# Performance work log

Measured on AMD Instinct MI355X. Metric: run time of the kernel, lower is better.

Reference implementation:

```python
import jax, jax.numpy as jnp
import numpy as np

D_PROJ = 256      # core d_proj
WIN = 1536        # win_small (mid path, L<=mid_thr)
STRIDE = 384      # stride_small


def setup_inputs() -> dict:
    key = jax.random.key(0)
    ks = jax.random.split(key, 6)
    B, L, d_h, T, d_g = 4, 8192, 1024, 512, 256
    H = jax.random.normal(ks[0], (B, L, d_h), jnp.float32)
    G = jax.random.normal(ks[1], (B, T, d_g), jnp.float32)
    attn_mask = jnp.ones((B, L), dtype=bool)
    Wq_core = jax.random.normal(ks[2], (d_g, D_PROJ), jnp.float32) / np.float32(np.sqrt(d_g))
    Wk_core = jax.random.normal(ks[3], (d_h, D_PROJ), jnp.float32) / np.float32(np.sqrt(d_h))
    Wq_win = jax.random.normal(ks[4], (d_g, d_h), jnp.float32) / np.float32(np.sqrt(d_g))
    Wk_win = jax.random.normal(ks[5], (d_h, d_h), jnp.float32) / np.float32(np.sqrt(d_h))
    return dict(H=H, G=G, attn_mask=attn_mask, Wq_core=Wq_core, Wk_core=Wk_core,
                Wq_win=Wq_win, Wk_win=Wk_win)


def _core_pool(Hk, G, mask, Wq_core, Wk_core):
    # GoSpecificWattiPooling: GO-query cross-attention pooling over residues.
    q = jnp.einsum('btg,gp->btp', G, Wq_core)                 # [B,T,P]
    k = jnp.einsum('bwd,dp->bwp', Hk, Wk_core)                # [B,W,P]
    scores = jnp.einsum('btp,bwp->btw', q, k) * (D_PROJ ** -0.5)
    scores = jnp.where(mask[:, None, :], scores, jnp.float32(-1e30))
    alpha = jax.nn.softmax(scores, axis=-1)                   # over residues
    return jnp.einsum('btw,bwd->btd', alpha, Hk)              # [B,T,d_h]


def _window_starts(L, win, stride):
    starts, s = [], 0
    while s < L:
        e = min(s + win, L)
        starts.append(s)
        if e == L:
            break
        s += stride
    return starts


def reference(H, G, attn_mask, Wq_core, Wk_core, Wq_win, Wk_win):
    B, L, D = H.shape
    T = G.shape[1]
    starts = jnp.asarray(_window_starts(L, WIN, STRIDE), jnp.int32)
    q_t = jnp.einsum('btg,gd->btd', G, Wq_win)                # [B,T,D]
    scale = D ** -0.5

    def step(carry, s0):
        m, ssum, z = carry
        Hk = jax.lax.dynamic_slice_in_dim(H, s0, WIN, axis=1)
        mk = jax.lax.dynamic_slice_in_dim(attn_mask, s0, WIN, axis=1)
        Zk = _core_pool(Hk, G, mk, Wq_core, Wk_core)          # [B,T,D]
        k_w = jnp.einsum('btd,de->bte', Zk, Wk_win)
        lw = (jnp.sum(q_t * k_w, axis=-1, keepdims=True) * scale).astype(jnp.float32)
        m_new = jnp.maximum(m, lw)
        exp_m = jnp.exp(m - m_new)
        exp_w = jnp.exp(lw - m_new)
        ssum = ssum * exp_m + exp_w
        z = z * exp_m + exp_w * Zk.astype(jnp.float32)
        return (m_new, ssum, z), None

    init = (jnp.full((B, T, 1), -jnp.inf, jnp.float32),
            jnp.zeros((B, T, 1), jnp.float32),
            jnp.zeros((B, T, D), jnp.float32))
    (m, ssum, z), _ = jax.lax.scan(step, init, starts)
    return (z / (ssum + 1e-8)).astype(H.dtype)
```

## Files before the change

### kernel.cpp

```cpp
#include <hip/hip_runtime.h>
#include <math.h>

constexpr int Bb = 4;
constexpr int Lb = 8192;
constexpr int Dh = 1024;
constexpr int Tt = 512;
constexpr int Dg = 256;
constexpr int Pp = 256;
constexpr int NW = 19;

typedef unsigned short u16;
typedef __bf16 bf16x8 __attribute__((ext_vector_type(8)));
typedef float f32x4 __attribute__((ext_vector_type(4)));
typedef unsigned short us8 __attribute__((ext_vector_type(8)));

__device__ __forceinline__ u16 f2bf(float x) {
  union { float f; unsigned u; } v;
  v.f = x;
  unsigned r = v.u + 0x7FFFu + ((v.u >> 16) & 1u);
  return (u16)(r >> 16);
}
__device__ __forceinline__ float bf2f(unsigned v) {
  union { unsigned u; float f; } c;
  c.u = v << 16;
  return c.f;
}

#define GLDS16(g, l)                                                          \
  __builtin_amdgcn_global_load_lds(                                           \
      (const __attribute__((address_space(1))) void*)(g),                     \
      (__attribute__((address_space(3))) void*)(l), 16, 0, 0)

__device__ __forceinline__ void stage_ops(const u16* __restrict__ A, int lda,
                                          int bm, int kA, u16* As,
                                          const u16* __restrict__ B, int ldb,
                                          int bn, int kB, u16* Bs, int tid,
                                          int wid) {
  const int rr = tid >> 3;
  const int c16 = (tid & 7) ^ (rr & 7);
#pragma unroll
  for (int cc = 0; cc < 4; cc++) {
    const int r = cc * 64 + rr;
    GLDS16(A + (long long)(bm + r) * lda + kA + c16 * 8,
           As + cc * 4096 + wid * 512);
  }
#pragma unroll
  for (int cc = 0; cc < 4; cc++) {
    const int r = cc * 64 + rr;
    GLDS16(B + (long long)(bn + r) * ldb + kB + c16 * 8,
           Bs + cc * 4096 + wid * 512);
  }
}

template <int OB>
__global__ __launch_bounds__(512, 1) void gemm256(const u16* __restrict__ A,
                                                  const u16* __restrict__ B,
                                                  void* __restrict__ C,
                                                  int K, int lda, int ldb,
                                                  int ldc, long long sA,
                                                  long long sB, long long sC,
                                                  long long sK, int kSplit,
                                                  float alpha) {
  __shared__ u16 lds[65536];

  const int gx = gridDim.x, gy = gridDim.y;
  int flat = blockIdx.x + gx * (blockIdx.y + gy * blockIdx.z);
  const int nwg = gx * gy * (int)gridDim.z;
  const int q = nwg >> 3, r = nwg & 7;
  const int xcd = flat & 7, sub = flat >> 3;
  flat = (xcd < r ? xcd * (q + 1) : r * (q + 1) + (xcd - r) * q) + sub;
  const int bmI = flat % gx;
  const int t1 = flat / gx;
  const int bnI = t1 % gy;
  const int z = t1 / gy;

  const int b = z / kSplit, ks = z % kSplit;
  const int kLen = K / kSplit;
  const int nt = kLen >> 6;
  A += b * sA + (long long)ks * kLen;
  B += b * sB + (long long)ks * kLen;
  const long long cOff = (long long)b * sC + (long long)ks * sK;

  const int bm = bmI * 256, bn = bnI * 256;
  const int tid = threadIdx.x;
  const int wid = tid >> 6, l = tid & 63;
  const int wm = wid >> 2, wn = wid & 3;
  const int rl = l & 15, kq = l >> 4;
  const int xr = rl & 7;

  f32x4 acc[8][4];
#pragma unroll
  for (int i = 0; i < 8; i++)
#pragma unroll
    for (int j = 0; j < 4; j++) acc[i][j] = (f32x4){0.f, 0.f, 0.f, 0.f};

  stage_ops(A, lda, bm, 0, lds, B, ldb, bn, 0, lds + 32768, tid, wid);
  stage_ops(A, lda, bm, 64, lds + 16384, B, ldb, bn, 64, lds + 49152, tid, wid);
  asm volatile("s_waitcnt vmcnt(8)" ::: "memory");
  __builtin_amdgcn_s_barrier();

  for (int t = 0; t < nt; t++) {
    const int cur = t & 1;
    const u16* As = lds + cur * 16384;
    const u16* Bs = lds + 32768 + cur * 16384;
    bf16x8 a0[4][2], bb[4][2];

#pragma unroll
    for (int i = 0; i < 4; i++)
#pragma unroll
      for (int s = 0; s < 2; s++)
        a0[i][s] = *(const bf16x8*)(As + (wm * 128 + i * 16 + rl) * 64 +
                                    (((s * 4 + kq) ^ xr) << 3));
#pragma unroll
    for (int j = 0; j < 2; j++)
#pragma unroll
      for (int s = 0; s < 2; s++)
        bb[j][s] = *(const bf16x8*)(Bs + (wn * 64 + j * 16 + rl) * 64 +
                                    (((s * 4 + kq) ^ xr) << 3));
    __builtin_amdgcn_s_barrier();
    __builtin_amdgcn_s_setprio(1);
#pragma unroll
    for (int i = 0; i < 4; i++)
#pragma unroll
      for (int j = 0; j < 2; j++)
#pragma unroll
        for (int s = 0; s < 2; s++)
          acc[i][j] = __builtin_amdgcn_mfma_f32_16x16x32_bf16(
              a0[i][s], bb[j][s], acc[i][j], 0, 0, 0);
    __builtin_amdgcn_s_setprio(0);
    __builtin_amdgcn_s_barrier();

#pragma unroll
    for (int j = 2; j < 4; j++)
#pragma unroll
      for (int s = 0; s < 2; s++)
        bb[j][s] = *(const bf16x8*)(Bs + (wn * 64 + j * 16 + rl) * 64 +
                                    (((s * 4 + kq) ^ xr) << 3));
    __builtin_amdgcn_s_barrier();
    __builtin_amdgcn_s_setprio(1);
#pragma unroll
    for (int i = 0; i < 4; i++)
#pragma unroll
      for (int j = 2; j < 4; j++)
#pragma unroll
        for (int s = 0; s < 2; s++)
          acc[i][j] = __builtin_amdgcn_mfma_f32_16x16x32_bf16(
              a0[i][s], bb[j][s], acc[i][j], 0, 0, 0);
    __builtin_amdgcn_s_setprio(0);
    __builtin_amdgcn_s_barrier();

#pragma unroll
    for (int i = 0; i < 4; i++)
#pragma unroll
      for (int s = 0; s < 2; s++)
        a0[i][s] = *(const bf16x8*)(As + (wm * 128 + 64 + i * 16 + rl) * 64 +
                                    (((s * 4 + kq) ^ xr) << 3));
    __builtin_amdgcn_s_barrier();
    __builtin_amdgcn_s_setprio(1);
#pragma unroll
    for (int i = 0; i < 4; i++)
#pragma unroll
      for (int j = 2; j < 4; j++)
#pragma unroll
        for (int s = 0; s < 2; s++)
          acc[i + 4][j] = __builtin_amdgcn_mfma_f32_16x16x32_bf16(
              a0[i][s], bb[j][s], acc[i + 4][j], 0, 0, 0);
    __builtin_amdgcn_s_setprio(0);
    __builtin_amdgcn_s_barrier();

    if (t + 2 < nt) {
      u16* Asw = (u16*)lds + cur * 16384;
      u16* Bsw = (u16*)lds + 32768 + cur * 16384;
      stage_ops(A, lda, bm, (t + 2) * 64, Asw, B, ldb, bn, (t + 2) * 64, Bsw,
                tid, wid);
    }
    __builtin_amdgcn_s_setprio(1);
#pragma unroll
    for (int i = 0; i < 4; i++)
#pragma unroll
      for (int j = 0; j < 2; j++)
#pragma unroll
        for (int s = 0; s < 2; s++)
          acc[i + 4][j] = __builtin_amdgcn_mfma_f32_16x16x32_bf16(
              a0[i][s], bb[j][s], acc[i + 4][j], 0, 0, 0);
    __builtin_amdgcn_s_setprio(0);
    if (t + 2 < nt)
      asm volatile("s_waitcnt vmcnt(8)" ::: "memory");
    else
      asm volatile("s_waitcnt vmcnt(0)" ::: "memory");
    __builtin_amdgcn_s_barrier();
  }

  float* Cf = (float*)C;
  u16* Cb = (u16*)C;
#pragma unroll
  for (int i = 0; i < 8; i++) {
    const int row0 = bm + wm * 128 + i * 16 + kq * 4;
#pragma unroll
    for (int j = 0; j < 4; j++) {
      const int col = bn + wn * 64 + j * 16 + rl;
#pragma unroll
      for (int r2 = 0; r2 < 4; r2++) {
        const float v = alpha * acc[i][j][r2];
        const long long idx = cOff + (long long)(row0 + r2) * ldc + col;
        if (OB)
          Cb[idx] = f2bf(v);
        else
          Cf[idx] = v;
      }
    }
  }
}

template <int OB, int ORD>
__global__ __launch_bounds__(256) void mgemm(const u16* __restrict__ A,
                                             const u16* __restrict__ B,
                                             void* __restrict__ C,
                                             int K, int lda, int ldb, int ldc,
                                             long long sA, long long sB,
                                             long long sC, long long sK,
                                             int kSplit, float alpha) {
  __shared__ u16 smem[8192];
  u16* As = smem;
  u16* Bs = smem + 4096;

  const int gx = gridDim.x, gy = gridDim.y;
  int flat = blockIdx.x + gx * (blockIdx.y + gy * blockIdx.z);
  const int nwg = gx * gy * (int)gridDim.z;
  const int q = nwg >> 3, r = nwg & 7;
  const int xcd = flat & 7, sub = flat >> 3;
  flat = (xcd < r ? xcd * (q + 1) : r * (q + 1) + (xcd - r) * q) + sub;
  int bmI, bnI, z;
  if (ORD == 0) {
    bmI = flat % gx;
    const int t = flat / gx;
    bnI = t % gy;
    z = t / gy;
  } else {
    bnI = flat % gy;
    const int t = flat / gy;
    bmI = t % gx;
    z = t / gx;
  }

  const int b = z / kSplit, ks = z % kSplit;
  const int kLen = K / kSplit;
  A += b * sA + (long long)ks * kLen;
  B += b * sB + (long long)ks * kLen;
  const long long cOff = (long long)b * sC + (long long)ks * sK;

  const int bm = bmI * 128;
  const int bn = bnI * 128;
  const int tid = threadIdx.x;
  const int l = tid & 63;
  const int wid = tid >> 6;
  const int wm = wid >> 1, wn = wid & 1;

  const int sr = l >> 2, sj = l & 3;
  const int skb = sj ^ ((sr >> 1) & 3);

  f32x4 acc[4][4];
#pragma unroll
  for (int i = 0; i < 4; i++)
#pragma unroll
    for (int j = 0; j < 4; j++) acc[i][j] = (f32x4){0.f, 0.f, 0.f, 0.f};

  const int rl = l & 15, kb = l >> 4;

  for (int k0 = 0; k0 < kLen; k0 += 32) {
    __syncthreads();
    {
      const int c1 = wid, c2 = wid + 4;
      GLDS16(A + (long long)(bm + c1 * 16 + sr) * lda + k0 + skb * 8,
             As + c1 * 512);
      GLDS16(A + (long long)(bm + c2 * 16 + sr) * lda + k0 + skb * 8,
             As + c2 * 512);
      GLDS16(B + (long long)(bn + c1 * 16 + sr) * ldb + k0 + skb * 8,
             Bs + c1 * 512);
      GLDS16(B + (long long)(bn + c2 * 16 + sr) * ldb + k0 + skb * 8,
             Bs + c2 * 512);
    }
    __syncthreads();

    bf16x8 af[4], bfr[4];
#pragma unroll
    for (int f = 0; f < 4; f++) {
      const int rowA = wm * 64 + f * 16 + rl;
      const int unitA = rowA * 4 + (kb ^ ((rowA >> 1) & 3));
      af[f] = *(const bf16x8*)(As + unitA * 8);
      const int rowB = wn * 64 + f * 16 + rl;
      const int unitB = rowB * 4 + (kb ^ ((rowB >> 1) & 3));
      bfr[f] = *(const bf16x8*)(Bs + unitB * 8);
    }
#pragma unroll
    for (int i = 0; i < 4; i++)
#pragma unroll
      for (int j = 0; j < 4; j++)
        acc[i][j] = __builtin_amdgcn_mfma_f32_16x16x32_bf16(af[i], bfr[j],
                                                            acc[i][j], 0, 0, 0);
  }

  float* Cf = (float*)C;
  u16* Cb = (u16*)C;
#pragma unroll
  for (int i = 0; i < 4; i++) {
    const int row0 = bm + wm * 64 + i * 16 + (l >> 4) * 4;
#pragma unroll
    for (int j = 0; j < 4; j++) {
      const int col = bn + wn * 64 + j * 16 + (l & 15);
#pragma unroll
      for (int r2 = 0; r2 < 4; r2++) {
        const float v = alpha * acc[i][j][r2];
        const long long idx = cOff + (long long)(row0 + r2) * ldc + col;
        if (OB)
          Cb[idx] = f2bf(v);
        else
          Cf[idx] = v;
      }
    }
  }
}

__global__ __launch_bounds__(256) void convk(const float* __restrict__ in,
                                             u16* __restrict__ out, long long n4) {
  for (long long i = (long long)blockIdx.x * 256 + threadIdx.x; i < n4;
       i += (long long)gridDim.x * 256) {
    const float4 v = ((const float4*)in)[i];
    ushort4 o;
    o.x = f2bf(v.x);
    o.y = f2bf(v.y);
    o.z = f2bf(v.z);
    o.w = f2bf(v.w);
    ((ushort4*)out)[i] = o;
  }
}

__global__ __launch_bounds__(256) void convT3(const float* __restrict__ in,
                                              u16* __restrict__ outR,
                                              u16* __restrict__ outT) {
  __shared__ float t[64][65];
  const int b = blockIdx.z;
  const float* ib = in + (long long)b * Lb * Dh;
  u16* oR = outR + (long long)b * Lb * Dh;
  u16* oT = outT + (long long)b * Dh * Lb;
  const int r0 = blockIdx.x * 64, c0 = blockIdx.y * 64;
  const int tid = threadIdx.x;

  const int lr = tid >> 2;
  const int lc = (tid & 3) * 16;
  u16 tmp[16];
#pragma unroll
  for (int j = 0; j < 4; j++) {
    const float4 v =
        *(const float4*)(ib + (long long)(r0 + lr) * Dh + c0 + lc + j * 4);
    *(float4*)&t[lr][lc + j * 4] = v;
    tmp[j * 4 + 0] = f2bf(v.x);
    tmp[j * 4 + 1] = f2bf(v.y);
    tmp[j * 4 + 2] = f2bf(v.z);
    tmp[j * 4 + 3] = f2bf(v.w);
  }
  *(us8*)(oR + (long long)(r0 + lr) * Dh + c0 + lc) = *(us8*)&tmp[0];
  *(us8*)(oR + (long long)(r0 + lr) * Dh + c0 + lc + 8) = *(us8*)&tmp[8];
  __syncthreads();

  const int dr = tid >> 2;
  const int ll = (tid & 3) * 16;
  u16 tt[16];
#pragma unroll
  for (int j = 0; j < 16; j++) tt[j] = f2bf(t[ll + j][dr]);
  *(us8*)(oT + (long long)(c0 + dr) * Lb + r0 + ll) = *(us8*)&tt[0];
  *(us8*)(oT + (long long)(c0 + dr) * Lb + r0 + ll + 8) = *(us8*)&tt[8];
}

__global__ __launch_bounds__(256) void t32(const float* __restrict__ in,
                                           u16* __restrict__ out, int R, int C,
                                           long long sIn, long long sOut) {
  __shared__ float t[32][33];
  const int b = blockIdx.z;
  in += (long long)b * sIn;
  out += (long long)b * sOut;
  const int r0 = blockIdx.x * 32, c0 = blockIdx.y * 32;
  const int tx = threadIdx.x, ty = threadIdx.y;
#pragma unroll
  for (int i = 0; i < 4; i++)
    t[ty + i * 8][tx] = in[(long long)(r0 + ty + i * 8) * C + c0 + tx];
  __syncthreads();
#pragma unroll
  for (int i = 0; i < 4; i++)
    out[(long long)(c0 + ty + i * 8) * R + r0 + tx] = f2bf(t[tx][ty + i * 8]);
}

__global__ __launch_bounds__(256) void addout8(const float* __restrict__ p,
                                               float* __restrict__ out, long long n4) {
  for (long long i = (long long)blockIdx.x * 256 + threadIdx.x; i < n4;
       i += (long long)gridDim.x * 256) {
    float4 s = ((const float4*)p)[i];
#pragma unroll
    for (int j = 1; j < 8; j++) {
      const float4 v = ((const float4*)p)[i + (long long)j * n4];
      s.x += v.x;
      s.y += v.y;
      s.z += v.z;
      s.w += v.w;
    }
    ((float4*)out)[i] = s;
  }
}

__global__ __launch_bounds__(256) void combine2(const u16* __restrict__ S,
                                                const u16* __restrict__ V,
                                                u16* __restrict__ Gm) {
  __shared__ u16 Ss[Lb];
  __shared__ float mx_s[64], se_s[64], sv_s[64], coef_s[64];
  __shared__ float m_s[NW], cw_s[NW];

  const int bt = blockIdx.x;
  const u16* Srow = S + (long long)bt * Lb;
  const u16* Vrow = V + (long long)bt * Lb;
  u16* Grow = Gm + (long long)bt * Lb;

  const int tid = threadIdx.x;
  const int ln = tid & 63;
  const int wid = tid >> 6;

  for (int i = tid; i < Lb / 8; i += 256) {
    ((uint4*)Ss)[i] = ((const uint4*)Srow)[i];
  }
  __syncthreads();

  for (int i = 0; i < 16; i++) {
    const int c = wid * 16 + i;
    const int j0 = c * 128 + ln * 2;
    const unsigned sp = *(const unsigned*)&Ss[j0];
    const float s0 = bf2f(sp & 0xffffu), s1 = bf2f(sp >> 16);
    float mx = fmaxf(s0, s1);
#pragma unroll
    for (int o = 32; o; o >>= 1) mx = fmaxf(mx, __shfl_xor(mx, o, 64));
    const unsigned vv = *(const unsigned*)(Vrow + j0);
    const float v0 = bf2f(vv & 0xffffu), v1 = bf2f(vv >> 16);
    const float e0 = __expf(s0 - mx), e1 = __expf(s1 - mx);
    float se = e0 + e1;
    float sv = e0 * v0 + e1 * v1;
#pragma unroll
    for (int o = 32; o; o >>= 1) {
      se += __shfl_xor(se, o, 64);
      sv += __shfl_xor(sv, o, 64);
    }
    if (ln == 0) {
      mx_s[c] = mx;
      se_s[c] = se;
      sv_s[c] = sv;
    }
  }
  __syncthreads();

  if (wid == 0) {
    float lw = -1e30f, mw = 0.f, dw = 1.f;
    if (ln < NW) {
      const int c0 = (ln == 18) ? 52 : 3 * ln;
      mw = -1e30f;
#pragma unroll
      for (int k = 0; k < 12; k++) mw = fmaxf(mw, mx_s[c0 + k]);
      float d = 0.f, n = 0.f;
#pragma unroll
      for (int k = 0; k < 12; k++) {
        const float r = __expf(mx_s[c0 + k] - mw);
        d = fmaf(se_s[c0 + k], r, d);
        n = fmaf(sv_s[c0 + k], r, n);
      }
      dw = d;
      lw = (n / d) * 0.03125f;
    }
    float M = lw;
#pragma unroll
    for (int o = 32; o; o >>= 1) M = fmaxf(M, __shfl_xor(M, o, 64));
    const float e = (ln < NW) ? __expf(lw - M) : 0.f;
    float ss = e;
#pragma unroll
    for (int o = 32; o; o >>= 1) ss += __shfl_xor(ss, o, 64);
    if (ln < NW) {
      m_s[ln] = mw;
      cw_s[ln] = e / (ss + 1e-8f) / dw;
    }
  }
  __syncthreads();

  if (tid < 64) {
    const int c = tid;
    const int wlo = (c <= 11) ? 0 : (c - 9) / 3;
    const int whi = min(17, c / 3);
    const float mx = mx_s[c];
    float cf = 0.f;
    for (int w = wlo; w <= whi; w++) cf = fmaf(cw_s[w], __expf(mx - m_s[w]), cf);
    if (c >= 52) cf = fmaf(cw_s[18], __expf(mx - m_s[18]), cf);
    coef_s[c] = cf;
  }
  __syncthreads();

  for (int i = tid; i < Lb / 8; i += 256) {
    const int l0 = i * 8;
    const int c = l0 >> 7;
    const float mx = mx_s[c], cf = coef_s[c];
    const us8 sp = *(const us8*)&Ss[l0];
    us8 o;
#pragma unroll
    for (int j = 0; j < 8; j++)
      o[j] = f2bf(__expf(bf2f((unsigned)sp[j]) - mx) * cf);
    *(us8*)(Grow + l0) = o;
  }
}

extern "C" void kernel_launch(void* const* d_in, const int* in_sizes, int n_in,
                              void* d_out, int out_size, void* d_ws, size_t ws_size,
                              hipStream_t stream) {
  const float* H = (const float*)d_in[0];
  const float* G = (const float*)d_in[1];
  const float* Wq_core = (const float*)d_in[3];
  const float* Wk_core = (const float*)d_in[4];
  const float* Wq_win = (const float*)d_in[5];
  const float* Wk_win = (const float*)d_in[6];
  float* out = (float*)d_out;

  const size_t MB = (size_t)1 << 20;
  char* w = (char*)d_ws;
  u16* Hb    = (u16*)(w);
  u16* gb    = (u16*)(w);
  u16* HTb   = (u16*)(w + 64 * MB);
  u16* Sb    = (u16*)(w + 128 * MB);
  float* part = (float*)(w + 128 * MB);
  u16* Kfb   = (u16*)(w + 192 * MB);
  u16* Vb    = (u16*)(w + 192 * MB);
  u16* qb    = (u16*)(w + 208 * MB);
  u16* qtb   = (u16*)(w + 209 * MB);
  u16* Wkwb  = (u16*)(w + 213 * MB);
  u16* WkcTb = (u16*)(w + 215 * MB);
  u16* WqcTb = (u16*)(w + 215 * MB + MB / 2);
  u16* WqwTb = (u16*)(w + 216 * MB);
  u16* Gb    = (u16*)(w + 217 * MB);
  u16* ub    = (u16*)(w + 224 * MB);

  convT3<<<dim3(Lb / 64, Dh / 64, Bb), 256, 0, stream>>>(H, Hb, HTb);
  t32<<<dim3(32, 8, 1), dim3(32, 8), 0, stream>>>(Wk_core, WkcTb, Dh, Pp, 0, 0);
  t32<<<dim3(8, 8, 1), dim3(32, 8), 0, stream>>>(Wq_core, WqcTb, Dg, Pp, 0, 0);
  t32<<<dim3(8, 32, 1), dim3(32, 8), 0, stream>>>(Wq_win, WqwTb, Dg, Dh, 0, 0);
  convk<<<1024, 256, 0, stream>>>(Wk_win, Wkwb, (long long)Dh * Dh / 4);
  convk<<<512, 256, 0, stream>>>(G, Gb, (long long)Bb * Tt * Dg / 4);

  gemm256<1><<<dim3(128, 1, 1), 512, 0, stream>>>(
      Hb, WkcTb, Kfb, Dh, Dh, Dh, Pp, 0, 0, 0, 0, 1, 1.f);

  mgemm<1, 0><<<dim3(16, 2, 1), 256, 0, stream>>>(
      Gb, WqcTb, qb, Dg, Dg, Dg, Pp, 0, 0, 0, 0, 1, 1.f);

  mgemm<1, 0><<<dim3(16, 8, 1), 256, 0, stream>>>(
      Gb, WqwTb, qtb, Dg, Dg, Dg, Dh, 0, 0, 0, 0, 1, 1.f);

  mgemm<1, 0><<<dim3(16, 8, 1), 256, 0, stream>>>(
      qtb, Wkwb, ub, Dh, Dh, Dh, Dh, 0, 0, 0, 0, 1, 1.f);

  gemm256<1><<<dim3(2, 32, Bb), 512, 0, stream>>>(
      qb, Kfb, Sb, Pp, Pp, Pp, Lb, (long long)Tt * Pp, (long long)Lb * Pp,
      (long long)Tt * Lb, 0, 1, 0.0625f);

  gemm256<1><<<dim3(2, 32, Bb), 512, 0, stream>>>(
      ub, Hb, Vb, Dh, Dh, Dh, Lb, (long long)Tt * Dh, (long long)Lb * Dh,
      (long long)Tt * Lb, 0, 1, 1.f);

  combine2<<<dim3(Bb * Tt), 256, 0, stream>>>(Sb, Vb, gb);

  gemm256<0><<<dim3(2, 4, Bb * 8), 512, 0, stream>>>(
      gb, HTb, part, Lb, Lb, Lb, Dh, (long long)Tt * Lb, (long long)Dh * Lb,
      (long long)Tt * Dh, (long long)Bb * Tt * Dh, 8, 1.f);

  addout8<<<2048, 256, 0, stream>>>(part, out, (long long)Bb * Tt * Dh / 4);
}
```

Before: 296.9 us.

## Drop transposed H copy; read row-major B via registers in final GEMM

Removes the convT3 kernel that wrote both a bf16 copy and a transposed bf16 copy of H, and replaces it with a plain conversion. This cuts one full-size bf16 write of H and the costly transpose. The final split-K GEMM becomes a new gemm256rb kernel that loads B row-major into registers and scatters it transposed and swizzled into LDS, while A still uses direct global-to-LDS loads. The trade-off is extra register pressure and scalar LDS stores inside the GEMM main loop, which could slow that GEMM.

```diff
diff --git a/kernel.cpp b/kernel.cpp
--- a/kernel.cpp
+++ b/kernel.cpp
@@ -31,25 +31,26 @@
       (const __attribute__((address_space(1))) void*)(g),                     \
       (__attribute__((address_space(3))) void*)(l), 16, 0, 0)
 
+__device__ __forceinline__ void stage_A(const u16* __restrict__ A, int lda,
+                                        int bm, int kA, u16* As, int tid,
+                                        int wid) {
+  const int rr = tid >> 3;
+  const int c16 = (tid & 7) ^ (rr & 7);
+#pragma unroll
+  for (int cc = 0; cc < 4; cc++) {
+    const int r = cc * 64 + rr;
+    GLDS16(A + (long long)(bm + r) * lda + kA + c16 * 8,
+           As + cc * 4096 + wid * 512);
+  }
+}
+
 __device__ __forceinline__ void stage_ops(const u16* __restrict__ A, int lda,
                                           int bm, int kA, u16* As,
                                           const u16* __restrict__ B, int ldb,
                                           int bn, int kB, u16* Bs, int tid,
                                           int wid) {
-  const int rr = tid >> 3;
-  const int c16 = (tid & 7) ^ (rr & 7);
-#pragma unroll
-  for (int cc = 0; cc < 4; cc++) {
-    const int r = cc * 64 + rr;
-    GLDS16(A + (long long)(bm + r) * lda + kA + c16 * 8,
-           As + cc * 4096 + wid * 512);
-  }
-#pragma unroll
-  for (int cc = 0; cc < 4; cc++) {
-    const int r = cc * 64 + rr;
-    GLDS16(B + (long long)(bn + r) * ldb + kB + c16 * 8,
-           Bs + cc * 4096 + wid * 512);
-  }
+  stage_A(A, lda, bm, kA, As, tid, wid);
+  stage_A(B, ldb, bn, kB, Bs, tid, wid);
 }
 
 template <int OB>
@@ -207,6 +208,196 @@
           Cb[idx] = f2bf(v);
         else
           Cf[idx] = v;
+      }
+    }
+  }
+}
+
+__global__ __launch_bounds__(512, 1) void gemm256rb(const u16* __restrict__ A,
+                                                    const u16* __restrict__ B,
+                                                    float* __restrict__ C,
+                                                    int K, int lda, int ldb,
+                                                    int ldc, long long sA,
+                                                    long long sB, long long sC,
+                                                    long long sK, int kSplit,
+                                                    float alpha) {
+  __shared__ u16 lds[65536];
+
+  const int gx = gridDim.x, gy = gridDim.y;
+  int flat = blockIdx.x + gx * (blockIdx.y + gy * blockIdx.z);
+  const int nwg = gx * gy * (int)gridDim.z;
+  const int q = nwg >> 3, r = nwg & 7;
+  const int xcd = flat & 7, sub = flat >> 3;
+  flat = (xcd < r ? xcd * (q + 1) : r * (q + 1) + (xcd - r) * q) + sub;
+  const int bmI = flat % gx;
+  const int t1 = flat / gx;
+  const int bnI = t1 % gy;
+  const int z = t1 / gy;
+
+  const int b = z / kSplit, ks = z % kSplit;
+  const int kLen = K / kSplit;
+  const int nt = kLen >> 6;
+  A += b * sA + (long long)ks * kLen;
+  B += b * sB + (long long)ks * kLen * (long long)ldb;
+  const long long cOff = (long long)b * sC + (long long)ks * sK;
+
+  const int bm = bmI * 256, bn = bnI * 256;
+  const int tid = threadIdx.x;
+  const int wid = tid >> 6, l = tid & 63;
+  const int wm = wid >> 2, wn = wid & 3;
+  const int rl = l & 15, kq = l >> 4;
+  const int xr = rl & 7;
+
+  const int bk = tid & 63;
+  const int bj = (tid >> 6) * 4;
+  const int bku = bk >> 3, bkl = bk & 7;
+
+  f32x4 acc[8][4];
+#pragma unroll
+  for (int i = 0; i < 8; i++)
+#pragma unroll
+    for (int j = 0; j < 4; j++) acc[i][j] = (f32x4){0.f, 0.f, 0.f, 0.f};
+
+  us8 br0[4], br1[4], breg[4];
+#pragma unroll
+  for (int c = 0; c < 4; c++)
+    br0[c] = *(const us8*)(B + (long long)(0 * 64 + bk) * ldb + bn + (bj + c) * 8);
+#pragma unroll
+  for (int c = 0; c < 4; c++)
+    br1[c] = *(const us8*)(B + (long long)(1 * 64 + bk) * ldb + bn + (bj + c) * 8);
+  stage_A(A, lda, bm, 0, lds, tid, wid);
+  stage_A(A, lda, bm, 64, lds + 16384, tid, wid);
+  asm volatile("s_waitcnt vmcnt(8)" ::: "memory");
+  {
+    u16* B0 = (u16*)lds + 32768;
+    u16* B1 = (u16*)lds + 49152;
+#pragma unroll
+    for (int c = 0; c < 4; c++)
+#pragma unroll
+      for (int i = 0; i < 8; i++) {
+        const int nn = 8 * (bj + c) + i;
+        const int off = nn * 64 + ((bku ^ i) << 3) + bkl;
+        B0[off] = br0[c][i];
+        B1[off] = br1[c][i];
+      }
+  }
+  asm volatile("s_waitcnt vmcnt(0) lgkmcnt(0)" ::: "memory");
+  __builtin_amdgcn_s_barrier();
+
+  for (int t = 0; t < nt; t++) {
+    const int cur = t & 1;
+    const u16* As = lds + cur * 16384;
+    const u16* Bs = lds + 32768 + cur * 16384;
+    bf16x8 a0[4][2], bb[4][2];
+
+    if (t + 2 < nt) {
+#pragma unroll
+      for (int c = 0; c < 4; c++)
+        breg[c] = *(const us8*)(B + (long long)((t + 2) * 64 + bk) * ldb + bn +
+                                (bj + c) * 8);
+    }
+#pragma unroll
+    for (int i = 0; i < 4; i++)
+#pragma unroll
+      for (int s = 0; s < 2; s++)
+        a0[i][s] = *(const bf16x8*)(As + (wm * 128 + i * 16 + rl) * 64 +
+                                    (((s * 4 + kq) ^ xr) << 3));
+#pragma unroll
+    for (int j = 0; j < 2; j++)
+#pragma unroll
+      for (int s = 0; s < 2; s++)
+        bb[j][s] = *(const bf16x8*)(Bs + (wn * 64 + j * 16 + rl) * 64 +
+                                    (((s * 4 + kq) ^ xr) << 3));
+    __builtin_amdgcn_s_barrier();
+    __builtin_amdgcn_s_setprio(1);
+#pragma unroll
+    for (int i = 0; i < 4; i++)
+#pragma unroll
+      for (int j = 0; j < 2; j++)
+#pragma unroll
+        for (int s = 0; s < 2; s++)
+          acc[i][j] = __builtin_amdgcn_mfma_f32_16x16x32_bf16(
+              a0[i][s], bb[j][s], acc[i][j], 0, 0, 0);
+    __builtin_amdgcn_s_setprio(0);
+    __builtin_amdgcn_s_barrier();
+
+#pragma unroll
+    for (int j = 2; j < 4; j++)
+#pragma unroll
+      for (int s = 0; s < 2; s++)
+        bb[j][s] = *(const bf16x8*)(Bs + (wn * 64 + j * 16 + rl) * 64 +
+                                    (((s * 4 + kq) ^ xr) << 3));
+    __builtin_amdgcn_s_barrier();
+    __builtin_amdgcn_s_setprio(1);
+#pragma unroll
+    for (int i = 0; i < 4; i++)
+#pragma unroll
+      for (int j = 2; j < 4; j++)
+#pragma unroll
+        for (int s = 0; s < 2; s++)
+          acc[i][j] = __builtin_amdgcn_mfma_f32_16x16x32_bf16(
+              a0[i][s], bb[j][s], acc[i][j], 0, 0, 0);
+    __builtin_amdgcn_s_setprio(0);
+    __builtin_amdgcn_s_barrier();
+
+#pragma unroll
+    for (int i = 0; i < 4; i++)
+#pragma unroll
+      for (int s = 0; s < 2; s++)
+        a0[i][s] = *(const bf16x8*)(As + (wm * 128 + 64 + i * 16 + rl) * 64 +
+                                    (((s * 4 + kq) ^ xr) << 3));
+    __builtin_amdgcn_s_barrier();
+    __builtin_amdgcn_s_setprio(1);
+#pragma unroll
+    for (int i = 0; i < 4; i++)
+#pragma unroll
+      for (int j = 2; j < 4; j++)
+#pragma unroll
+        for (int s = 0; s < 2; s++)
+          acc[i + 4][j] = __builtin_amdgcn_mfma_f32_16x16x32_bf16(
+              a0[i][s], bb[j][s], acc[i + 4][j], 0, 0, 0);
+    __builtin_amdgcn_s_setprio(0);
+    __builtin_amdgcn_s_barrier();
+
+    if (t + 2 < nt)
+      stage_A(A, lda, bm, (t + 2) * 64, (u16*)lds + cur * 16384, tid, wid);
+    __builtin_amdgcn_s_setprio(1);
+#pragma unroll
+    for (int i = 0; i < 4; i++)
+#pragma unroll
+      for (int j = 0; j < 2; j++)
+#pragma unroll
+        for (int s = 0; s < 2; s++)
+          acc[i + 4][j] = __builtin_amdgcn_mfma_f32_16x16x32_bf16(
+              a0[i][s], bb[j][s], acc[i + 4][j], 0, 0, 0);
+    __builtin_amdgcn_s_setprio(0);
+    if (t + 2 < nt) {
+      asm volatile("s_waitcnt vmcnt(4)" ::: "memory");
+      u16* Bw = (u16*)lds + 32768 + cur * 16384;
+#pragma unroll
+      for (int c = 0; c < 4; c++)
+#pragma unroll
+        for (int i = 0; i < 8; i++) {
+          const int nn = 8 * (bj + c) + i;
+          Bw[nn * 64 + ((bku ^ i) << 3) + bkl] = breg[c][i];
+        }
+      asm volatile("s_waitcnt lgkmcnt(0)" ::: "memory");
+    } else {
+      asm volatile("s_waitcnt vmcnt(0)" ::: "memory");
+    }
+    __builtin_amdgcn_s_barrier();
+  }
+
+#pragma unroll
+  for (int i = 0; i < 8; i++) {
+    const int row0 = bm + wm * 128 + i * 16 + kq * 4;
+#pragma unroll
+    for (int j = 0; j < 4; j++) {
+      const int col = bn + wn * 64 + j * 16 + rl;
+#pragma unroll
+      for (int r2 = 0; r2 < 4; r2++) {
+        const long long idx = cOff + (long long)(row0 + r2) * ldc + col;
+        C[idx] = alpha * acc[i][j][r2];
       }
     }
   }
@@ -335,43 +526,6 @@
   }
 }
 
-__global__ __launch_bounds__(256) void convT3(const float* __restrict__ in,
-                                              u16* __restrict__ outR,
-                                              u16* __restrict__ outT) {
-  __shared__ float t[64][65];
-  const int b = blockIdx.z;
-  const float* ib = in + (long long)b * Lb * Dh;
-  u16* oR = outR + (long long)b * Lb * Dh;
-  u16* oT = outT + (long long)b * Dh * Lb;
-  const int r0 = blockIdx.x * 64, c0 = blockIdx.y * 64;
-  const int tid = threadIdx.x;
-
-  const int lr = tid >> 2;
-  const int lc = (tid & 3) * 16;
-  u16 tmp[16];
-#pragma unroll
-  for (int j = 0; j < 4; j++) {
-    const float4 v =
-        *(const float4*)(ib + (long long)(r0 + lr) * Dh + c0 + lc + j * 4);
-    *(float4*)&t[lr][lc + j * 4] = v;
-    tmp[j * 4 + 0] = f2bf(v.x);
-    tmp[j * 4 + 1] = f2bf(v.y);
-    tmp[j * 4 + 2] = f2bf(v.z);
-    tmp[j * 4 + 3] = f2bf(v.w);
-  }
-  *(us8*)(oR + (long long)(r0 + lr) * Dh + c0 + lc) = *(us8*)&tmp[0];
-  *(us8*)(oR + (long long)(r0 + lr) * Dh + c0 + lc + 8) = *(us8*)&tmp[8];
-  __syncthreads();
-
-  const int dr = tid >> 2;
-  const int ll = (tid & 3) * 16;
-  u16 tt[16];
-#pragma unroll
-  for (int j = 0; j < 16; j++) tt[j] = f2bf(t[ll + j][dr]);
-  *(us8*)(oT + (long long)(c0 + dr) * Lb + r0 + ll) = *(us8*)&tt[0];
-  *(us8*)(oT + (long long)(c0 + dr) * Lb + r0 + ll + 8) = *(us8*)&tt[8];
-}
-
 __global__ __launch_bounds__(256) void t32(const float* __restrict__ in,
                                            u16* __restrict__ out, int R, int C,
                                            long long sIn, long long sOut) {
@@ -524,8 +678,7 @@
   const size_t MB = (size_t)1 << 20;
   char* w = (char*)d_ws;
   u16* Hb    = (u16*)(w);
-  u16* gb    = (u16*)(w);
-  u16* HTb   = (u16*)(w + 64 * MB);
+  u16* gb    = (u16*)(w + 64 * MB);
   u16* Sb    = (u16*)(w + 128 * MB);
   float* part = (float*)(w + 128 * MB);
   u16* Kfb   = (u16*)(w + 192 * MB);
@@ -539,7 +692,7 @@
   u16* Gb    = (u16*)(w + 217 * MB);
   u16* ub    = (u16*)(w + 224 * MB);
 
-  convT3<<<dim3(Lb / 64, Dh / 64, Bb), 256, 0, stream>>>(H, Hb, HTb);
+  convk<<<2048, 256, 0, stream>>>(H, Hb, (long long)Bb * Lb * Dh / 4);
   t32<<<dim3(32, 8, 1), dim3(32, 8), 0, stream>>>(Wk_core, WkcTb, Dh, Pp, 0, 0);
   t32<<<dim3(8, 8, 1), dim3(32, 8), 0, stream>>>(Wq_core, WqcTb, Dg, Pp, 0, 0);
   t32<<<dim3(8, 32, 1), dim3(32, 8), 0, stream>>>(Wq_win, WqwTb, Dg, Dh, 0, 0);
@@ -568,8 +721,8 @@
 
   combine2<<<dim3(Bb * Tt), 256, 0, stream>>>(Sb, Vb, gb);
 
-  gemm256<0><<<dim3(2, 4, Bb * 8), 512, 0, stream>>>(
-      gb, HTb, part, Lb, Lb, Lb, Dh, (long long)Tt * Lb, (long long)Dh * Lb,
+  gemm256rb<<<dim3(2, 4, Bb * 8), 512, 0, stream>>>(
+      gb, Hb, part, Lb, Lb, Dh, Dh, (long long)Tt * Lb, (long long)Lb * Dh,
       (long long)Tt * Dh, (long long)Bb * Tt * Dh, 8, 1.f);
 
   addout8<<<2048, 256, 0, stream>>>(part, out, (long long)Bb * Tt * Dh / 4);
```

After: 281.9 us. -5.0%, faster.
